# Optimization experiments

Hardware: AMD Instinct MI355X
Metric: run time of the kernel (lower is better)

The kernel has to match this reference:

```python
import jax, jax.numpy as jnp
import numpy as np

IN_C = 32
OUT_C = 64
K = 6
B = 16
N = 2048


def _mk_linear(key, fan_in, fan_out):
    kw, kb = jax.random.split(key)
    lim = 1.0 / np.sqrt(fan_in)
    W = jax.random.uniform(kw, (fan_in, fan_out), jnp.float32, -lim, lim)
    b = jax.random.uniform(kb, (fan_out,), jnp.float32, -lim, lim)
    return W, b


def setup_inputs() -> dict:
    key = jax.random.key(0)
    ks = jax.random.split(key, 7)
    x = jax.random.normal(ks[0], (B * N, IN_C), jnp.float32)
    batch = jnp.repeat(jnp.arange(B, dtype=jnp.int32), N)
    # conv0: 2*IN_C -> OUT_C -> OUT_C
    W1_0, b1_0 = _mk_linear(ks[1], 2 * IN_C, OUT_C)
    W2_0, b2_0 = _mk_linear(ks[2], OUT_C, OUT_C)
    # conv1: 2*OUT_C -> OUT_C//2 -> OUT_C//2
    W1_1, b1_1 = _mk_linear(ks[3], 2 * OUT_C, OUT_C // 2)
    W2_1, b2_1 = _mk_linear(ks[4], OUT_C // 2, OUT_C // 2)
    # conv2: 2*(OUT_C//2) -> OUT_C -> OUT_C
    W1_2, b1_2 = _mk_linear(ks[5], OUT_C, OUT_C)
    W2_2, b2_2 = _mk_linear(ks[6], OUT_C, OUT_C)
    return dict(x=x, batch=batch,
                W1_0=W1_0, b1_0=b1_0, W2_0=W2_0, b2_0=b2_0,
                W1_1=W1_1, b1_1=b1_1, W2_1=W2_1, b2_1=b2_1,
                W1_2=W1_2, b1_2=b1_2, W2_2=W2_2, b2_2=b2_2)


def _dynamic_edge_conv(xf, W1, b1, W2, b2, Bn, Nn):
    # xf: [Bn*Nn, C] node features; graphs are equal-size contiguous blocks
    C = xf.shape[-1]
    xb = xf.reshape(Bn, Nn, C)
    # pairwise squared distances within each graph: [Bn, Nn, Nn]
    sq = jnp.sum(xb * xb, axis=-1)
    d2 = sq[:, :, None] + sq[:, None, :] - 2.0 * jnp.einsum('bnc,bmc->bnm', xb, xb)
    # exclude self-loops (loop=False in knn_graph)
    d2 = d2 + jnp.eye(Nn, dtype=xf.dtype) * jnp.float32(1e9)
    # k nearest neighbors per node: [Bn, Nn, K]
    _, idx = jax.lax.top_k(-d2, K)
    # gather neighbor features x_j: [Bn, Nn, K, C]
    xj = jax.vmap(lambda xg, ig: xg[ig])(xb, idx)
    xi = xb[:, :, None, :]
    # message = MLP(concat[x_i, x_j - x_i]); aggr = max over neighbors
    msg = jnp.concatenate([jnp.broadcast_to(xi, xj.shape), xj - xi], axis=-1)
    h = jax.nn.relu(msg @ W1 + b1) @ W2 + b2
    out = jnp.max(h, axis=2)  # [Bn, Nn, out]
    return out.reshape(Bn * Nn, -1)


def reference(x, batch, W1_0, b1_0, W2_0, b2_0, W1_1, b1_1, W2_1, b2_1, W1_2, b1_2, W2_2, b2_2):
    Bn = int(np.asarray(batch)[-1]) + 1
    Nn = x.shape[0] // Bn
    x0 = jax.nn.relu(_dynamic_edge_conv(x, W1_0, b1_0, W2_0, b2_0, Bn, Nn))
    x1 = jax.nn.relu(_dynamic_edge_conv(x0, W1_1, b1_1, W2_1, b2_1, Bn, Nn))
    x2 = _dynamic_edge_conv(x1, W1_2, b1_2, W2_2, b2_2, Bn, Nn) + x0
    return jax.nn.relu(x2)
```

## Files before the change

kernel.cpp:

```cpp
#include <hip/hip_runtime.h>

#define NB   16
#define NN   2048
#define NPTS (NB * NN)
#define KNB  6

typedef __attribute__((ext_vector_type(8))) short short8;
typedef __attribute__((ext_vector_type(2))) float f32x2;
typedef __attribute__((ext_vector_type(4))) float f32x4;
typedef __attribute__((ext_vector_type(16))) float f32x16;
typedef const __attribute__((address_space(4))) float cfloat;
typedef const __attribute__((address_space(4))) f32x2 cf32x2;

__device__ __forceinline__ unsigned bf16_rne(float f) {
    unsigned u = __float_as_uint(f);
    return (u + 0x7fffu + ((u >> 16) & 1u)) >> 16;
}

__global__ void prep_w(const float* __restrict__ W10, const float* __restrict__ W11,
                       const float* __restrict__ W12,
                       unsigned short* __restrict__ Whi0, unsigned short* __restrict__ Wlo0,
                       unsigned short* __restrict__ Whi1, unsigned short* __restrict__ Wlo1,
                       unsigned short* __restrict__ Whi2, unsigned short* __restrict__ Wlo2) {
    int t = blockIdx.x * 256 + threadIdx.x;
    if (t >= 4096) return;
    {
        const int n = t >> 5, k = t & 31;
        float v0, v2;
        if (n < 64) { v0 = W10[k * 64 + n] - W10[(32 + k) * 64 + n];
                      v2 = W12[k * 64 + n] - W12[(32 + k) * 64 + n]; }
        else        { v0 = W10[(32 + k) * 64 + (n - 64)];
                      v2 = W12[(32 + k) * 64 + (n - 64)]; }
        unsigned h0 = bf16_rne(v0);
        Whi0[t] = (unsigned short)h0;
        Wlo0[t] = (unsigned short)bf16_rne(v0 - __uint_as_float(h0 << 16));
        unsigned h2 = bf16_rne(v2);
        Whi2[t] = (unsigned short)h2;
        Wlo2[t] = (unsigned short)bf16_rne(v2 - __uint_as_float(h2 << 16));
    }
    {
        const int n = t >> 6, k = t & 63;
        float v;
        if (n < 32) v = W11[k * 32 + n] - W11[(64 + k) * 32 + n];
        else        v = W11[(64 + k) * 32 + (n - 32)];
        unsigned h = bf16_rne(v);
        Whi1[t] = (unsigned short)h;
        Wlo1[t] = (unsigned short)bf16_rne(v - __uint_as_float(h << 16));
    }
}

template<int C, int COUT>
__global__ __launch_bounds__(256, 2)
void prep_gemm(const float* __restrict__ x,
               const unsigned short* __restrict__ Whi,
               const unsigned short* __restrict__ Wlo,
               const float* __restrict__ b1,
               unsigned short* __restrict__ Xhi,
               unsigned short* __restrict__ Xlo,
               float* __restrict__ sq, float* __restrict__ AB) {
    constexpr int KT  = C / 16;
    constexpr int N2  = 2 * COUT;
    constexpr int NCT = N2 / 32;
    constexpr int RPB = 4 / NCT;
    constexpr int PPB = RPB * 32;
    constexpr int TPP = 256 / PPB;
    constexpr int Q   = C / TPP;
    const int tid = threadIdx.x;
    const int bid = blockIdx.x;

    {
        const int slot = tid & (TPP - 1);
        const int i    = bid * PPB + tid / TPP;
        float r[Q];
        const float4* rp = (const float4*)(x + (size_t)i * C + slot * Q);
#pragma unroll
        for (int c4 = 0; c4 < Q / 4; ++c4) {
            float4 f = rp[c4];
            r[4 * c4] = f.x; r[4 * c4 + 1] = f.y; r[4 * c4 + 2] = f.z; r[4 * c4 + 3] = f.w;
        }
        float s = 0.f;
#pragma unroll
        for (int c = 0; c < Q; ++c) s = fmaf(r[c], r[c], s);
#pragma unroll
        for (int d = 1; d < TPP; d <<= 1) s += __shfl_xor(s, d);
        if (slot == 0) sq[i] = s;

#pragma unroll
        for (int cc = 0; cc < Q; cc += 4) {
            unsigned uh0, uh1, ul0, ul1;
            {
                const unsigned h0 = bf16_rne(r[cc]);
                const unsigned h1 = bf16_rne(r[cc + 1]);
                const unsigned h2 = bf16_rne(r[cc + 2]);
                const unsigned h3 = bf16_rne(r[cc + 3]);
                const unsigned l0 = bf16_rne(r[cc]     - __uint_as_float(h0 << 16));
                const unsigned l1 = bf16_rne(r[cc + 1] - __uint_as_float(h1 << 16));
                const unsigned l2 = bf16_rne(r[cc + 2] - __uint_as_float(h2 << 16));
                const unsigned l3 = bf16_rne(r[cc + 3] - __uint_as_float(h3 << 16));
                uh0 = h0 | (h1 << 16); uh1 = h2 | (h3 << 16);
                ul0 = l0 | (l1 << 16); ul1 = l2 | (l3 << 16);
            }
            const size_t off = (size_t)i * C + slot * Q + cc;
            *(uint2*)(Xhi + off) = make_uint2(uh0, uh1);
            *(uint2*)(Xlo + off) = make_uint2(ul0, ul1);
        }
    }
    __syncthreads();

    const int w    = __builtin_amdgcn_readfirstlane(tid >> 6);
    const int lane = tid & 63;
    const int n31  = lane & 31;
    const int lh   = lane >> 5;
    const int rt   = bid * RPB + w / NCT;
    const int ct   = w % NCT;
    const int p0   = rt * 32;

    short8 ah[KT], al[KT], wh[KT], wl[KT];
#pragma unroll
    for (int kt = 0; kt < KT; ++kt) {
        const size_t poff = (size_t)(p0 + n31) * C + kt * 16 + lh * 8;
        ah[kt] = *(const short8*)(Xhi + poff);
        al[kt] = *(const short8*)(Xlo + poff);
        const size_t woff = (size_t)(ct * 32 + n31) * C + kt * 16 + lh * 8;
        wh[kt] = *(const short8*)(Whi + woff);
        wl[kt] = *(const short8*)(Wlo + woff);
    }

    f32x16 acc = {0.f};
#pragma unroll
    for (int kt = 0; kt < KT; ++kt) {
        acc = __builtin_amdgcn_mfma_f32_32x32x16_bf16(ah[kt], wh[kt], acc, 0, 0, 0);
        acc = __builtin_amdgcn_mfma_f32_32x32x16_bf16(ah[kt], wl[kt], acc, 0, 0, 0);
        acc = __builtin_amdgcn_mfma_f32_32x32x16_bf16(al[kt], wh[kt], acc, 0, 0, 0);
    }

    const int nc = ct * 32 + n31;
    const float bias = (ct < COUT / 32) ? b1[nc] : 0.f;
#pragma unroll
    for (int r = 0; r < 16; ++r) {
        const int pt = p0 + (r & 3) + 8 * (r >> 2) + 4 * lh;
        AB[(size_t)pt * N2 + nc] = acc[r] + bias;
    }
}

__device__ __forceinline__ void insert6f(float s, float* dl) {
#pragma unroll
    for (int k = 0; k < 6; ++k) {
        const float a = dl[k];
        dl[k] = fminf(s, a);
        s = fmaxf(s, a);
    }
}

template<int C>
__global__ __launch_bounds__(256, 4)
void knn_scan(const unsigned short* __restrict__ Xhi,
              const unsigned short* __restrict__ Xlo,
              const float* __restrict__ sqv,
              unsigned* __restrict__ plist) {
    constexpr int KT    = C / 16;
    constexpr int SR    = C / 4;
    constexpr int ROWB  = SR * 16;
    constexpr int STEPB = 32 * ROWB;
    constexpr int LPT   = STEPB / 16 / 256;
    __shared__ __align__(16) char sm[3 * STEPB];

    const int tid  = threadIdx.x;
    const int w    = __builtin_amdgcn_readfirstlane(tid >> 6);
    const int bid  = blockIdx.x;
    const int swz  = ((bid & 7) << 7) | (bid >> 3);
    const int b    = swz >> 6;
    const int sp   = (swz >> 4) & 3;
    const int qg   = swz & 15;
    const int qt   = qg * 4 + w;
    const int lane = tid & 63;
    const int q31  = lane & 31;
    const int lh   = lane >> 5;
    const int base = b * NN;
    const int qloc = qt * 32 + q31;

    short8 bh[KT], bl[KT];
#pragma unroll
    for (int kt = 0; kt < KT; ++kt) {
        const size_t off = (size_t)(base + qloc) * C + kt * 16 + lh * 8;
        bh[kt] = *(const short8*)(Xhi + off);
        bl[kt] = *(const short8*)(Xlo + off);
    }

    float dl[6];
#pragma unroll
    for (int k = 0; k < 6; ++k) dl[k] = 1e30f;

    const int jbeg   = sp * (NN / 4);
    const int selfjb = qt * 32;

    const unsigned short* src[LPT];
#pragma unroll
    for (int l = 0; l < LPT; ++l) {
        const int sidx = tid + l * 256;
        const int row  = sidx / SR;
        const int slot = sidx % SR;
        const int u    = slot ^ (row & (SR - 1));
        const unsigned short* bp = (u < SR / 2) ? Xhi : Xlo;
        src[l] = bp + (size_t)(base + jbeg + row) * C + (u & (SR / 2 - 1)) * 8;
    }

    const int m       = q31 & (SR - 1);
    const int rowbase = q31 * ROWB;
    const float* sqp  = sqv + base + jbeg + lh * 4;
    float4 s4[4];

#define STAGE(BUF) do {                                                        \
    _Pragma("unroll")                                                          \
    for (int l = 0; l < LPT; ++l) {                                            \
        __builtin_amdgcn_global_load_lds(                                      \
            (const __attribute__((address_space(1))) void*)src[l],             \
            (__attribute__((address_space(3))) void*)                          \
                (sm + (BUF) * STEPB + l * 4096 + w * 1024),                    \
            16, 0, 0);                                                         \
        src[l] += 32 * C;                                                      \
    }                                                                          \
} while (0)

#define COMPUTE(BUF, JB) do {                                                  \
    const char* smc = sm + (BUF) * STEPB;                                      \
    f32x16 acc = {0.f};                                                        \
    _Pragma("unroll")                                                          \
    for (int kt = 0; kt < KT; ++kt) {                                          \
        const int uh = kt * 2 + lh;                                            \
        const int ul = 2 * KT + kt * 2 + lh;                                   \
        const short8 ah = *(const short8*)(smc + rowbase + ((uh ^ m) << 4));   \
        const short8 al = *(const short8*)(smc + rowbase + ((ul ^ m) << 4));   \
        acc = __builtin_amdgcn_mfma_f32_32x32x16_bf16(ah, bh[kt], acc, 0, 0, 0); \
        acc = __builtin_amdgcn_mfma_f32_32x32x16_bf16(ah, bl[kt], acc, 0, 0, 0); \
        acc = __builtin_amdgcn_mfma_f32_32x32x16_bf16(al, bh[kt], acc, 0, 0, 0); \
    }                                                                          \
    const unsigned ebase = (unsigned)(((JB) - jbeg) >> 1);        \
    const bool selfstep = ((JB) == selfjb);                                    \
    _Pragma("unroll")                                                          \
    for (int g4 = 0; g4 < 4; ++g4) {                                           \
        _Pragma("unroll")                                                      \
        for (int rr = 0; rr < 4; ++rr) {                                       \
            const int r = g4 * 4 + rr;                                         \
            float sc = fmaf(-2.f, acc[r],                                      \
                rr == 0 ? s4[g4].x : rr == 1 ? s4[g4].y :                      \
                rr == 2 ? s4[g4].z : s4[g4].w);                                \
            sc = __uint_as_float((__float_as_uint(sc) & 0xFFFFFF00u) |         \
                                 (ebase + (unsigned)((r & 3) + 4 * (r >> 2)))); \
            if (selfstep) {                                                    \
                const int rowr = (r & 3) + 8 * (r >> 2) + 4 * lh;              \
                sc = (rowr == q31) ? 1e30f : sc;                               \
            }                                                                  \
            insert6f(sc, dl);                                                  \
        }                                                                      \
    }                                                                          \
} while (0)

    STAGE(0);
    int jb = jbeg, cur = 0, nxt = 1;
#pragma unroll 1
    for (int st = 0; st < 15; ++st) {
#pragma unroll
        for (int g4 = 0; g4 < 4; ++g4) s4[g4] = *(const float4*)(sqp + g4 * 8);
        asm volatile("" ::: "memory");
        STAGE(nxt);
        if constexpr (C == 32) asm volatile("s_waitcnt vmcnt(5)" ::: "memory");
        else                   asm volatile("s_waitcnt vmcnt(6)" ::: "memory");
        __builtin_amdgcn_s_barrier();
        COMPUTE(cur, jb);
        jb += 32; sqp += 32;
        cur = nxt;
        nxt = (nxt == 2) ? 0 : nxt + 1;
    }
    {
#pragma unroll
        for (int g4 = 0; g4 < 4; ++g4) s4[g4] = *(const float4*)(sqp + g4 * 8);
        asm volatile("s_waitcnt vmcnt(0)" ::: "memory");
        __builtin_amdgcn_s_barrier();
        COMPUTE(cur, jb);
    }
#undef STAGE
#undef COMPUTE

    unsigned* o = plist + (size_t)(base + qloc) * 48 + (sp * 2 + lh) * 6;
#pragma unroll
    for (int k = 0; k < 6; ++k) {
        const unsigned bits = __float_as_uint(dl[k]);
        o[k] = bits ^ ((bits & 0x80000000u) ? 0xFFFFFFFFu : 0x80000000u);
    }
}

template<int C>
__global__ __launch_bounds__(256)
void rescore(const float* __restrict__ x, const float* __restrict__ sqv,
             const unsigned* __restrict__ plist, int* __restrict__ nbr) {
    const int bid  = blockIdx.x;
    const int bsw  = ((bid & 7) << 5) | (bid >> 3);
    const int gi   = bsw * 256 + threadIdx.x;
    const int i    = gi >> 1;
    const int slot = gi & 1;

    const unsigned* pr = plist + (size_t)i * 48 + slot * 24;

    unsigned long long best[7];
#pragma unroll
    for (int k = 0; k < 7; ++k) best[k] = ~0ull;
    for (int z4 = 0; z4 < 4; ++z4) {
        const unsigned* p = pr + z4 * 6;
        const unsigned zg = (unsigned)(slot * 4 + z4);
        for (int e = 0; e < 6; ++e) {
            unsigned long long v = ((unsigned long long)p[e] << 3) | zg;
            if (v >= best[6]) break;
            best[6] = v;
#pragma unroll
            for (int k = 5; k >= 0; --k) {
                if (best[k + 1] < best[k]) {
                    unsigned long long t = best[k]; best[k] = best[k + 1]; best[k + 1] = t;
                }
            }
        }
    }

    const int base = i & ~(NN - 1);
    float4 qv[C / 4];
    const float4* qp = (const float4*)(x + (size_t)i * C);
#pragma unroll
    for (int t = 0; t < C / 4; ++t) qv[t] = qp[t];

    unsigned long long out6[6];
#pragma unroll
    for (int k = 0; k < 6; ++k) out6[k] = ~0ull;

    for (int m = 0; m < 7; ++m) {
        const unsigned u32k = (unsigned)(best[m] >> 3);
        const int z = (int)(best[m] & 7ull);
        const unsigned orig = (u32k & 0x80000000u) ? (u32k ^ 0x80000000u) : ~u32k;
        const int e = (int)(orig & 255u);
        const int idx = e & 15;
        const int jloc = (z >> 1) * (NN / 4) + (e >> 4) * 32 +
                         (idx & 3) + 8 * (idx >> 2) + (z & 1) * 4;

        const float4* cp = (const float4*)(x + (size_t)(base + jloc) * C);
        float d0 = 0.f, d1 = 0.f, d2 = 0.f, d3 = 0.f;
#pragma unroll
        for (int t = 0; t < C / 4; ++t) {
            float4 a = cp[t];
            d0 = fmaf(a.x, qv[t].x, d0);
            d1 = fmaf(a.y, qv[t].y, d1);
            d2 = fmaf(a.z, qv[t].z, d2);
            d3 = fmaf(a.w, qv[t].w, d3);
        }
        const float s = fmaf(-2.f, (d0 + d1) + (d2 + d3), sqv[base + jloc]);
        unsigned u = __float_as_uint(s);
        u ^= (u & 0x80000000u) ? 0xFFFFFFFFu : 0x80000000u;
        unsigned long long key = ((unsigned long long)u << 11) | (unsigned)jloc;
#pragma unroll
        for (int k = 0; k < 6; ++k) {
            const unsigned long long ok = out6[k];
            const bool c = key < ok;
            out6[k] = c ? key : ok;
            key     = c ? ok  : key;
        }
    }

    unsigned long long fin[6];
#pragma unroll
    for (int k = 0; k < 6; ++k) fin[k] = out6[k];
#pragma unroll
    for (int k = 0; k < 6; ++k) {
        const unsigned long long v = out6[k];
        const unsigned lo = __shfl_xor((unsigned)v, 1);
        const unsigned hi = __shfl_xor((unsigned)(v >> 32), 1);
        unsigned long long key = ((unsigned long long)hi << 32) | lo;
#pragma unroll
        for (int q = 0; q < 6; ++q) {
            const unsigned long long ok = fin[q];
            const bool c = key < ok;
            fin[q] = c ? key : ok;
            key    = c ? ok  : key;
        }
    }
#pragma unroll
    for (int k = 0; k < 3; ++k)
        nbr[i * KNB + slot * 3 + k] = base + (int)(fin[slot * 3 + k] & 2047ull);
}

template<int COUT, bool RESID, int MINW>
__global__ __launch_bounds__(768, MINW)
void mlp_kernel(const float* __restrict__ AB, const int* __restrict__ nbr,
                const float* __restrict__ W2, const float* __restrict__ b2,
                const float* __restrict__ resid, float* __restrict__ out) {
    constexpr int HALF = COUT / 2;
    constexpr int NQ   = COUT / 4;
    constexpr int N2   = 2 * COUT;
    constexpr int RS = HALF + 4;
    __shared__ float Buf[2][3][64][RS];

    const int tid  = threadIdx.x;
    const int lane = tid & 63;
    const int wv   = __builtin_amdgcn_readfirstlane(tid >> 6);
    const int oh   = wv / 6;
    const int w6   = wv % 6;
    const int bid  = blockIdx.x;
    const int bsw  = ((bid & 7) << 6) | (bid >> 3);
    const int i    = bsw * 64 + lane;
    const int j    = nbr[i * KNB + w6];

    f32x2 uacc[HALF / 2];
#pragma unroll
    for (int o = 0; o < HALF / 2; ++o) uacc[o] = (f32x2){0.f, 0.f};

    cfloat* W2c = (cfloat*)(uintptr_t)W2;
    const float* Ap = AB + (size_t)i * N2;
    const float* Bp = AB + (size_t)j * N2 + COUT;

    const int qofs = (wv * 3) & (NQ - 1);

#pragma unroll 2
    for (int qi = 0; qi < NQ; ++qi) {
        const int oq = (qi + qofs) & (NQ - 1);
        const float4 a4 = *(const float4*)(Ap + 4 * oq);
        const float4 b4 = *(const float4*)(Bp + 4 * oq);
#pragma unroll
        for (int rr = 0; rr < 4; ++rr) {
            const int op = oq * 4 + rr;
            const float aop = rr == 0 ? a4.x : rr == 1 ? a4.y : rr == 2 ? a4.z : a4.w;
            const float bop = rr == 0 ? b4.x : rr == 1 ? b4.y : rr == 2 ? b4.z : b4.w;
            const float h = fmaxf(aop + bop, 0.f);
            cf32x2* w2p = (cf32x2*)(W2c + (size_t)op * COUT + oh * HALF);
            const f32x2 hv = {h, h};
#pragma unroll
            for (int o = 0; o < HALF / 2; ++o)
                uacc[o] += w2p[o] * hv;
        }
    }

    if (w6 >= 3) {
#pragma unroll
        for (int o = 0; o < HALF / 2; ++o) {
            Buf[oh][w6 - 3][lane][2 * o]     = uacc[o].x;
            Buf[oh][w6 - 3][lane][2 * o + 1] = uacc[o].y;
        }
    }
    __syncthreads();
    if (w6 < 3) {
#pragma unroll
        for (int o = 0; o < HALF / 2; ++o) {
            uacc[o].x = fmaxf(uacc[o].x, Buf[oh][w6][lane][2 * o]);
            uacc[o].y = fmaxf(uacc[o].y, Buf[oh][w6][lane][2 * o + 1]);
        }
    }
    __syncthreads();
    if (w6 == 1 || w6 == 2) {
#pragma unroll
        for (int o = 0; o < HALF / 2; ++o) {
            Buf[oh][w6][lane][2 * o]     = uacc[o].x;
            Buf[oh][w6][lane][2 * o + 1] = uacc[o].y;
        }
    }
    __syncthreads();
    if (w6 == 0) {
        float* po = out + (size_t)i * COUT + oh * HALF;
        const float* b2p = b2 + oh * HALF;
        const float* rp  = RESID ? (resid + (size_t)i * COUT + oh * HALF) : nullptr;
#pragma unroll
        for (int o = 0; o < HALF / 2; ++o) {
            float v0 = fmaxf(uacc[o].x,
                             fmaxf(Buf[oh][1][lane][2 * o], Buf[oh][2][lane][2 * o])) + b2p[2 * o];
            float v1 = fmaxf(uacc[o].y,
                             fmaxf(Buf[oh][1][lane][2 * o + 1], Buf[oh][2][lane][2 * o + 1])) + b2p[2 * o + 1];
            if (RESID) { v0 += rp[2 * o]; v1 += rp[2 * o + 1]; }
            po[2 * o]     = fmaxf(v0, 0.f);
            po[2 * o + 1] = fmaxf(v1, 0.f);
        }
    }
}

extern "C" void kernel_launch(void* const* d_in, const int* in_sizes, int n_in,
                              void* d_out, int out_size, void* d_ws, size_t ws_size,
                              hipStream_t stream) {
    const float* x    = (const float*)d_in[0];
    const float* W1_0 = (const float*)d_in[2];
    const float* b1_0 = (const float*)d_in[3];
    const float* W2_0 = (const float*)d_in[4];
    const float* b2_0 = (const float*)d_in[5];
    const float* W1_1 = (const float*)d_in[6];
    const float* b1_1 = (const float*)d_in[7];
    const float* W2_1 = (const float*)d_in[8];
    const float* b2_1 = (const float*)d_in[9];
    const float* W1_2 = (const float*)d_in[10];
    const float* b1_2 = (const float*)d_in[11];
    const float* W2_2 = (const float*)d_in[12];
    const float* b2_2 = (const float*)d_in[13];
    float* outp = (float*)d_out;

    unsigned* plist = (unsigned*)d_ws;
    float* x0  = (float*)(plist + (size_t)NPTS * 48);
    float* x1  = x0 + (size_t)NPTS * 64;
    float* sqb = x1 + (size_t)NPTS * 32;
    unsigned short* Whi0 = (unsigned short*)(sqb + NPTS);
    unsigned short* Wlo0 = Whi0 + 4096;
    unsigned short* Whi1 = Wlo0 + 4096;
    unsigned short* Wlo1 = Whi1 + 4096;
    unsigned short* Whi2 = Wlo1 + 4096;
    unsigned short* Wlo2 = Whi2 + 4096;
    unsigned short* Xhi = Wlo2 + 4096;
    unsigned short* Xlo = Xhi + (size_t)NPTS * 64;
    int* nbr = (int*)(Xlo + (size_t)NPTS * 64);
    float* AB = (float*)(nbr + (size_t)NPTS * KNB);

    const int rgrid  = NPTS * 2 / 256;
    const int scgrid = 1024;
    const int pgrid  = NPTS / 64;

    prep_w<<<16, 256, 0, stream>>>(W1_0, W1_1, W1_2, Whi0, Wlo0, Whi1, Wlo1, Whi2, Wlo2);

    prep_gemm<32, 64><<<NPTS / 32, 256, 0, stream>>>(x, Whi0, Wlo0, b1_0, Xhi, Xlo, sqb, AB);
    knn_scan<32><<<scgrid, 256, 0, stream>>>(Xhi, Xlo, sqb, plist);
    rescore<32><<<rgrid, 256, 0, stream>>>(x, sqb, plist, nbr);
    mlp_kernel<64, false, 5><<<pgrid, 768, 0, stream>>>(AB, nbr, W2_0, b2_0, nullptr, x0);

    prep_gemm<64, 32><<<NPTS / 64, 256, 0, stream>>>(x0, Whi1, Wlo1, b1_1, Xhi, Xlo, sqb, AB);
    knn_scan<64><<<scgrid, 256, 0, stream>>>(Xhi, Xlo, sqb, plist);
    rescore<64><<<rgrid, 256, 0, stream>>>(x0, sqb, plist, nbr);
    mlp_kernel<32, false, 4><<<pgrid, 768, 0, stream>>>(AB, nbr, W2_1, b2_1, nullptr, x1);

    prep_gemm<32, 64><<<NPTS / 32, 256, 0, stream>>>(x1, Whi2, Wlo2, b1_2, Xhi, Xlo, sqb, AB);
    knn_scan<32><<<scgrid, 256, 0, stream>>>(Xhi, Xlo, sqb, plist);
    rescore<32><<<rgrid, 256, 0, stream>>>(x1, sqb, plist, nbr);
    mlp_kernel<64, true, 5><<<pgrid, 768, 0, stream>>>(AB, nbr, W2_2, b2_2, x0, outp);
}
```

Before: 394.5 us.

## Fuse kNN rescore into MLP kernel, passing neighbor indices through LDS

Merges the rescore kernel into the edge MLP kernel. The first 128 threads of each 768-thread block do the candidate merge and exact rescoring for the block's 64 query points, then write neighbor indices to shared memory. This removes three kernel launches and the global nbr write and read. In exchange, the other 640 threads sit idle at a barrier during rescoring, and the min-waves-per-EU launch bounds are lowered, which may reduce occupancy.

New measurement: 386.9 us (median of 2 runs). About the same (-1.9%).

```diff
diff --git a/kernel.cpp b/kernel.cpp
--- a/kernel.cpp
+++ b/kernel.cpp
@@ -290,121 +290,120 @@
     }
 }
 
-template<int C>
-__global__ __launch_bounds__(256)
-void rescore(const float* __restrict__ x, const float* __restrict__ sqv,
-             const unsigned* __restrict__ plist, int* __restrict__ nbr) {
-    const int bid  = blockIdx.x;
-    const int bsw  = ((bid & 7) << 5) | (bid >> 3);
-    const int gi   = bsw * 256 + threadIdx.x;
-    const int i    = gi >> 1;
-    const int slot = gi & 1;
-
-    const unsigned* pr = plist + (size_t)i * 48 + slot * 24;
-
-    unsigned long long best[7];
-#pragma unroll
-    for (int k = 0; k < 7; ++k) best[k] = ~0ull;
-    for (int z4 = 0; z4 < 4; ++z4) {
-        const unsigned* p = pr + z4 * 6;
-        const unsigned zg = (unsigned)(slot * 4 + z4);
-        for (int e = 0; e < 6; ++e) {
-            unsigned long long v = ((unsigned long long)p[e] << 3) | zg;
-            if (v >= best[6]) break;
-            best[6] = v;
-#pragma unroll
-            for (int k = 5; k >= 0; --k) {
-                if (best[k + 1] < best[k]) {
-                    unsigned long long t = best[k]; best[k] = best[k + 1]; best[k + 1] = t;
-                }
-            }
-        }
-    }
-
-    const int base = i & ~(NN - 1);
-    float4 qv[C / 4];
-    const float4* qp = (const float4*)(x + (size_t)i * C);
-#pragma unroll
-    for (int t = 0; t < C / 4; ++t) qv[t] = qp[t];
-
-    unsigned long long out6[6];
-#pragma unroll
-    for (int k = 0; k < 6; ++k) out6[k] = ~0ull;
-
-    for (int m = 0; m < 7; ++m) {
-        const unsigned u32k = (unsigned)(best[m] >> 3);
-        const int z = (int)(best[m] & 7ull);
-        const unsigned orig = (u32k & 0x80000000u) ? (u32k ^ 0x80000000u) : ~u32k;
-        const int e = (int)(orig & 255u);
-        const int idx = e & 15;
-        const int jloc = (z >> 1) * (NN / 4) + (e >> 4) * 32 +
-                         (idx & 3) + 8 * (idx >> 2) + (z & 1) * 4;
-
-        const float4* cp = (const float4*)(x + (size_t)(base + jloc) * C);
-        float d0 = 0.f, d1 = 0.f, d2 = 0.f, d3 = 0.f;
-#pragma unroll
-        for (int t = 0; t < C / 4; ++t) {
-            float4 a = cp[t];
-            d0 = fmaf(a.x, qv[t].x, d0);
-            d1 = fmaf(a.y, qv[t].y, d1);
-            d2 = fmaf(a.z, qv[t].z, d2);
-            d3 = fmaf(a.w, qv[t].w, d3);
-        }
-        const float s = fmaf(-2.f, (d0 + d1) + (d2 + d3), sqv[base + jloc]);
-        unsigned u = __float_as_uint(s);
-        u ^= (u & 0x80000000u) ? 0xFFFFFFFFu : 0x80000000u;
-        unsigned long long key = ((unsigned long long)u << 11) | (unsigned)jloc;
-#pragma unroll
-        for (int k = 0; k < 6; ++k) {
-            const unsigned long long ok = out6[k];
-            const bool c = key < ok;
-            out6[k] = c ? key : ok;
-            key     = c ? ok  : key;
-        }
-    }
-
-    unsigned long long fin[6];
-#pragma unroll
-    for (int k = 0; k < 6; ++k) fin[k] = out6[k];
-#pragma unroll
-    for (int k = 0; k < 6; ++k) {
-        const unsigned long long v = out6[k];
-        const unsigned lo = __shfl_xor((unsigned)v, 1);
-        const unsigned hi = __shfl_xor((unsigned)(v >> 32), 1);
-        unsigned long long key = ((unsigned long long)hi << 32) | lo;
-#pragma unroll
-        for (int q = 0; q < 6; ++q) {
-            const unsigned long long ok = fin[q];
-            const bool c = key < ok;
-            fin[q] = c ? key : ok;
-            key    = c ? ok  : key;
-        }
-    }
-#pragma unroll
-    for (int k = 0; k < 3; ++k)
-        nbr[i * KNB + slot * 3 + k] = base + (int)(fin[slot * 3 + k] & 2047ull);
-}
-
-template<int COUT, bool RESID, int MINW>
+template<int C, int COUT, bool RESID, int MINW>
 __global__ __launch_bounds__(768, MINW)
-void mlp_kernel(const float* __restrict__ AB, const int* __restrict__ nbr,
-                const float* __restrict__ W2, const float* __restrict__ b2,
-                const float* __restrict__ resid, float* __restrict__ out) {
+void mlp_rescore(const float* __restrict__ x, const float* __restrict__ sqv,
+                 const unsigned* __restrict__ plist,
+                 const float* __restrict__ AB,
+                 const float* __restrict__ W2, const float* __restrict__ b2,
+                 const float* __restrict__ resid, float* __restrict__ out) {
     constexpr int HALF = COUT / 2;
     constexpr int NQ   = COUT / 4;
     constexpr int N2   = 2 * COUT;
     constexpr int RS = HALF + 4;
     __shared__ float Buf[2][3][64][RS];
+    __shared__ int nbrL[64][6];
 
     const int tid  = threadIdx.x;
     const int lane = tid & 63;
+    const int bid  = blockIdx.x;
+    const int bsw  = ((bid & 7) << 6) | (bid >> 3);
+    const int i    = bsw * 64 + lane;
+
+    if (tid < 128) {
+        const int ql   = tid >> 1;
+        const int qi   = bsw * 64 + ql;
+        const int slot = tid & 1;
+        const unsigned* pr = plist + (size_t)qi * 48 + slot * 24;
+
+        unsigned long long best[7];
+#pragma unroll
+        for (int k = 0; k < 7; ++k) best[k] = ~0ull;
+        for (int z4 = 0; z4 < 4; ++z4) {
+            const unsigned* p = pr + z4 * 6;
+            const unsigned zg = (unsigned)(slot * 4 + z4);
+            for (int e = 0; e < 6; ++e) {
+                unsigned long long v = ((unsigned long long)p[e] << 3) | zg;
+                if (v >= best[6]) break;
+                best[6] = v;
+#pragma unroll
+                for (int k = 5; k >= 0; --k) {
+                    if (best[k + 1] < best[k]) {
+                        unsigned long long t = best[k]; best[k] = best[k + 1]; best[k + 1] = t;
+                    }
+                }
+            }
+        }
+
+        const int base = qi & ~(NN - 1);
+        float4 qv[C / 4];
+        const float4* qp = (const float4*)(x + (size_t)qi * C);
+#pragma unroll
+        for (int t = 0; t < C / 4; ++t) qv[t] = qp[t];
+
+        unsigned long long out6[6];
+#pragma unroll
+        for (int k = 0; k < 6; ++k) out6[k] = ~0ull;
+
+        for (int mm = 0; mm < 7; ++mm) {
+            const unsigned u32k = (unsigned)(best[mm] >> 3);
+            const int z = (int)(best[mm] & 7ull);
+            const unsigned orig = (u32k & 0x80000000u) ? (u32k ^ 0x80000000u) : ~u32k;
+            const int e = (int)(orig & 255u);
+            const int idx = e & 15;
+            const int jloc = (z >> 1) * (NN / 4) + (e >> 4) * 32 +
+                             (idx & 3) + 8 * (idx >> 2) + (z & 1) * 4;
+
+            const float4* cp = (const float4*)(x + (size_t)(base + jloc) * C);
+            float d0 = 0.f, d1 = 0.f, d2 = 0.f, d3 = 0.f;
+#pragma unroll
+            for (int t = 0; t < C / 4; ++t) {
+                float4 a = cp[t];
+                d0 = fmaf(a.x, qv[t].x, d0);
+                d1 = fmaf(a.y, qv[t].y, d1);
+                d2 = fmaf(a.z, qv[t].z, d2);
+                d3 = fmaf(a.w, qv[t].w, d3);
+            }
+            const float s = fmaf(-2.f, (d0 + d1) + (d2 + d3), sqv[base + jloc]);
+            unsigned u = __float_as_uint(s);
+            u ^= (u & 0x80000000u) ? 0xFFFFFFFFu : 0x80000000u;
+            unsigned long long key = ((unsigned long long)u << 11) | (unsigned)jloc;
+#pragma unroll
+            for (int k = 0; k < 6; ++k) {
+                const unsigned long long ok = out6[k];
+                const bool c = key < ok;
+                out6[k] = c ? key : ok;
+                key     = c ? ok  : key;
+            }
+        }
+
+        unsigned long long fin[6];
+#pragma unroll
+        for (int k = 0; k < 6; ++k) fin[k] = out6[k];
+#pragma unroll
+        for (int k = 0; k < 6; ++k) {
+            const unsigned long long v = out6[k];
+            const unsigned lo = __shfl_xor((unsigned)v, 1);
+            const unsigned hi = __shfl_xor((unsigned)(v >> 32), 1);
+            unsigned long long key = ((unsigned long long)hi << 32) | lo;
+#pragma unroll
+            for (int q = 0; q < 6; ++q) {
+                const unsigned long long ok = fin[q];
+                const bool c = key < ok;
+                fin[q] = c ? key : ok;
+                key    = c ? ok  : key;
+            }
+        }
+#pragma unroll
+        for (int k = 0; k < 3; ++k)
+            nbrL[ql][slot * 3 + k] = base + (int)(fin[slot * 3 + k] & 2047ull);
+    }
+    __syncthreads();
+
     const int wv   = __builtin_amdgcn_readfirstlane(tid >> 6);
     const int oh   = wv / 6;
     const int w6   = wv % 6;
-    const int bid  = blockIdx.x;
-    const int bsw  = ((bid & 7) << 6) | (bid >> 3);
-    const int i    = bsw * 64 + lane;
-    const int j    = nbr[i * KNB + w6];
+    const int j    = nbrL[lane][w6];
 
     f32x2 uacc[HALF / 2];
 #pragma unroll
@@ -417,8 +416,8 @@
     const int qofs = (wv * 3) & (NQ - 1);
 
 #pragma unroll 2
-    for (int qi = 0; qi < NQ; ++qi) {
-        const int oq = (qi + qofs) & (NQ - 1);
+    for (int qi2 = 0; qi2 < NQ; ++qi2) {
+        const int oq = (qi2 + qofs) & (NQ - 1);
         const float4 a4 = *(const float4*)(Ap + 4 * oq);
         const float4 b4 = *(const float4*)(Bp + 4 * oq);
 #pragma unroll
@@ -506,10 +505,8 @@
     unsigned short* Wlo2 = Whi2 + 4096;
     unsigned short* Xhi = Wlo2 + 4096;
     unsigned short* Xlo = Xhi + (size_t)NPTS * 64;
-    int* nbr = (int*)(Xlo + (size_t)NPTS * 64);
-    float* AB = (float*)(nbr + (size_t)NPTS * KNB);
-
-    const int rgrid  = NPTS * 2 / 256;
+    float* AB = (float*)(Xlo + (size_t)NPTS * 64);
+
     const int scgrid = 1024;
     const int pgrid  = NPTS / 64;
 
@@ -517,16 +514,13 @@
 
     prep_gemm<32, 64><<<NPTS / 32, 256, 0, stream>>>(x, Whi0, Wlo0, b1_0, Xhi, Xlo, sqb, AB);
     knn_scan<32><<<scgrid, 256, 0, stream>>>(Xhi, Xlo, sqb, plist);
-    rescore<32><<<rgrid, 256, 0, stream>>>(x, sqb, plist, nbr);
-    mlp_kernel<64, false, 5><<<pgrid, 768, 0, stream>>>(AB, nbr, W2_0, b2_0, nullptr, x0);
+    mlp_rescore<32, 64, false, 4><<<pgrid, 768, 0, stream>>>(x, sqb, plist, AB, W2_0, b2_0, nullptr, x0);
 
     prep_gemm<64, 32><<<NPTS / 64, 256, 0, stream>>>(x0, Whi1, Wlo1, b1_1, Xhi, Xlo, sqb, AB);
     knn_scan<64><<<scgrid, 256, 0, stream>>>(Xhi, Xlo, sqb, plist);
-    rescore<64><<<rgrid, 256, 0, stream>>>(x0, sqb, plist, nbr);
-    mlp_kernel<32, false, 4><<<pgrid, 768, 0, stream>>>(AB, nbr, W2_1, b2_1, nullptr, x1);
+    mlp_rescore<64, 32, false, 3><<<pgrid, 768, 0, stream>>>(x0, sqb, plist, AB, W2_1, b2_1, nullptr, x1);
 
     prep_gemm<32, 64><<<NPTS / 32, 256, 0, stream>>>(x1, Whi2, Wlo2, b1_2, Xhi, Xlo, sqb, AB);
     knn_scan<32><<<scgrid, 256, 0, stream>>>(Xhi, Xlo, sqb, plist);
-    rescore<32><<<rgrid, 256, 0, stream>>>(x1, sqb, plist, nbr);
-    mlp_kernel<64, true, 5><<<pgrid, 768, 0, stream>>>(AB, nbr, W2_2, b2_2, x0, outp);
-}
+    mlp_rescore<32, 64, true, 4><<<pgrid, 768, 0, stream>>>(x1, sqb, plist, AB, W2_2, b2_2, x0, outp);
+}
```
